# Kernel optimization log

Hardware: AMD Instinct MI355X
Metric: run time of the kernel (lower is better)

The kernel has to match this reference:

```python
import jax, jax.numpy as jnp
import numpy as np

V, E, S, B, T = 100000, 64, 4, 2048, 200
D = 2 * E          # memory_vector_dim
C = E              # controller_units
CIN = 2 * E + D    # controller input: x_t (2E) + prev read (D)
P = 2 * (D + 1) + 2 * D  # (key+beta) for read & write heads + erase + add


def setup_inputs() -> dict:
    key = jax.random.key(0)
    ks = jax.random.split(key, 16)
    g = lambda k, sh, sc=0.05: jax.random.normal(k, sh, dtype=jnp.float32) * sc
    return {
        "item": jax.random.randint(ks[0], (B,), 0, V),
        "cate": jax.random.randint(ks[1], (B,), 0, V),
        "hist_item": jax.random.randint(ks[2], (B, T), 0, V),
        "hist_cate": jax.random.randint(ks[3], (B, T), 0, V),
        "mask": jnp.ones((B, T), jnp.float32),
        "embedding": g(ks[4], (V, E)),
        "gru_Wih": g(ks[5], (3 * C, CIN)),
        "gru_Whh": g(ks[6], (3 * C, C)),
        "gru_bih": jnp.zeros((3 * C,), jnp.float32),
        "gru_bhh": jnp.zeros((3 * C,), jnp.float32),
        "Wp": g(ks[7], (P, C)),
        "bp": jnp.zeros((P,), jnp.float32),
        "Wo": g(ks[8], (E, C + D)),
        "bo": jnp.zeros((E,), jnp.float32),
        "M0": g(ks[9], (S, D), 0.1),
        "fc1_w": g(ks[10], (200, 5 * E)),
        "fc1_b": jnp.zeros((200,), jnp.float32),
        "prelu1_a": jnp.full((1,), 0.25, jnp.float32),
        "fc2_w": g(ks[11], (80, 200)),
        "fc2_b": jnp.zeros((80,), jnp.float32),
        "prelu2_a": jnp.full((1,), 0.25, jnp.float32),
        "fc3_w": g(ks[12], (2, 80)),
        "fc3_b": jnp.zeros((2,), jnp.float32),
    }


def _cos_addr(k, beta, M):
    # content addressing: softmax(beta * cosine_sim(k, M))  k:[B,D] M:[B,S,D]
    kn = k / (jnp.linalg.norm(k, axis=-1, keepdims=True) + 1e-8)
    Mn = M / (jnp.linalg.norm(M, axis=-1, keepdims=True) + 1e-8)
    K = jnp.einsum('bd,bsd->bs', kn, Mn)
    return jax.nn.softmax(beta[:, None] * K, axis=-1)


def _prelu(x, a):
    return jnp.where(x > 0, x, a * x)


def _mimn_rnn(hist_emb, mask, gru_Wih, gru_Whh, gru_bih, gru_bhh, Wp, bp, Wo, bo, M0):
    Bn = hist_emb.shape[0]
    h0 = jnp.zeros((Bn, C), hist_emb.dtype)
    r0 = jnp.zeros((Bn, D), hist_emb.dtype)
    Mi = jnp.broadcast_to(M0[None], (Bn, S, D))

    def step(carry, inp):
        h, M, read = carry
        x_t, m_t = inp                      # x_t [B,2E], m_t [B]
        ctrl_in = jnp.concatenate([x_t, read], axis=-1)
        gi = ctrl_in @ gru_Wih.T + gru_bih
        gh = h @ gru_Whh.T + gru_bhh
        i_r, i_z, i_n = jnp.split(gi, 3, axis=-1)
        h_r, h_z, h_n = jnp.split(gh, 3, axis=-1)
        rg = jax.nn.sigmoid(i_r + h_r)
        zg = jax.nn.sigmoid(i_z + h_z)
        ng = jnp.tanh(i_n + rg * h_n)
        h_new = (1.0 - zg) * ng + zg * h
        # head parameters
        p = h_new @ Wp.T + bp               # [B, P]
        hp_r, hp_w = p[:, :D + 1], p[:, D + 1:2 * (D + 1)]
        erase = jax.nn.sigmoid(p[:, 2 * (D + 1):2 * (D + 1) + D])
        add = jnp.tanh(p[:, -D:])
        k_r, beta_r = jnp.tanh(hp_r[:, :D]), jax.nn.softplus(hp_r[:, D])
        k_w, beta_w = jnp.tanh(hp_w[:, :D]), jax.nn.softplus(hp_w[:, D])
        w_r = _cos_addr(k_r, beta_r, M)
        w_w = _cos_addr(k_w, beta_w, M)
        read_new = jnp.einsum('bs,bsd->bd', w_r, M)
        M_new = M * (1.0 - w_w[..., None] * erase[:, None, :]) + w_w[..., None] * add[:, None, :]
        out = jnp.concatenate([h_new, read_new], axis=-1) @ Wo.T + bo  # [B,E]
        # sequence-length masking (dynamic_rnn semantics)
        v = (m_t > 0)[:, None]
        h = jnp.where(v, h_new, h)
        read = jnp.where(v, read_new, read)
        M = jnp.where(v[..., None], M_new, M)
        out = jnp.where(v, out, jnp.zeros_like(out))
        return (h, M, read), out

    xs = (jnp.swapaxes(hist_emb, 0, 1), jnp.swapaxes(mask, 0, 1))  # [T,B,...]
    _, outs = jax.lax.scan(step, (h0, Mi, r0), xs)
    return jnp.swapaxes(outs, 0, 1)  # [B,T,E]


def reference(item, cate, hist_item, hist_cate, mask, embedding,
              gru_Wih, gru_Whh, gru_bih, gru_bhh, Wp, bp, Wo, bo, M0,
              fc1_w, fc1_b, prelu1_a, fc2_w, fc2_b, prelu2_a, fc3_w, fc3_b):
    item_emb = jnp.concatenate([embedding[item], embedding[cate]], axis=1)      # [B,2E]
    hist_emb = jnp.concatenate([embedding[hist_item], embedding[hist_cate]], axis=2)  # [B,T,2E]
    seq_len = mask.sum(1).astype(jnp.int32)
    outputs = _mimn_rnn(hist_emb, mask, gru_Wih, gru_Whh, gru_bih, gru_bhh, Wp, bp, Wo, bo, M0)
    last_out = jnp.take_along_axis(outputs, (seq_len - 1)[:, None, None], axis=1)[:, 0, :]
    hist_sum = (hist_emb * mask[..., None]).sum(1)                              # [B,2E]
    x = jnp.concatenate([item_emb, hist_sum, last_out], axis=1)                 # [B,5E]
    x = _prelu(x @ fc1_w.T + fc1_b, prelu1_a)
    x = _prelu(x @ fc2_w.T + fc2_b, prelu2_a)
    return x @ fc3_w.T + fc3_b
```

## Files before the change

### kernel.cpp

```cpp
#include <hip/hip_runtime.h>

#define VV 100000
#define BB 2048
#define TT 200
#define GG 192
#define PP 514
#define RPB 8

typedef _Float16 half8 __attribute__((ext_vector_type(8)));
typedef float floatx4 __attribute__((ext_vector_type(4)));
#define MFMA16(a, b, c) __builtin_amdgcn_mfma_f32_16x16x32_f16((a), (b), (c), 0, 0, 0)

#define BARRIER_LDS() do { \
    __asm__ volatile("s_waitcnt lgkmcnt(0)" ::: "memory"); \
    __builtin_amdgcn_s_barrier(); } while (0)

__device__ __forceinline__ float fsigm(float x) { return 1.0f / (1.0f + __expf(-x)); }
__device__ __forceinline__ float ftanh(float x) {
    float e = __expf(2.0f * x);
    return 1.0f - 2.0f / (e + 1.0f);
}
__device__ __forceinline__ float fsoftplus(float x) {
    float e = __expf(-fabsf(x));
    return fmaxf(x, 0.0f) + __logf(1.0f + e);
}

#define DPP_ADD(x, ctrl, rmask) \
    ((x) + __int_as_float(__builtin_amdgcn_update_dpp( \
        0, __float_as_int(x), (ctrl), (rmask), 0xf, true)))
__device__ __forceinline__ float wsum64(float x) {
    x = DPP_ADD(x, 0x111, 0xf);
    x = DPP_ADD(x, 0x112, 0xf);
    x = DPP_ADD(x, 0x114, 0xf);
    x = DPP_ADD(x, 0x118, 0xf);
    x = DPP_ADD(x, 0x142, 0xa);
    x = DPP_ADD(x, 0x143, 0xc);
    return __int_as_float(__builtin_amdgcn_readlane(__float_as_int(x), 63));
}
__device__ __forceinline__ float dot4(float4 w, float4 a) {
    return w.x * a.x + w.y * a.y + w.z * a.z + w.w * a.w;
}

__global__ __launch_bounds__(192) void build_tables(
    const float* __restrict__ emb,
    const float* __restrict__ Wih,
    const float* __restrict__ bih,
    float* __restrict__ GIi, float* __restrict__ GIc)
{
    __shared__ float sE[64 * 64];
    int tid = threadIdx.x;
    int v0 = blockIdx.x * 64;
    for (int i = tid; i < 64 * 64; i += 192) {
        int vv = i >> 6, k = i & 63;
        int gv = v0 + vv;
        sE[i] = (gv < VV) ? emb[(size_t)gv * 64 + k] : 0.0f;
    }
    __syncthreads();
    int n = tid;
    float bi = bih[n];
    {
        float4 w[16];
        const float4* wp = (const float4*)(Wih + n * 256);
#pragma unroll
        for (int q = 0; q < 16; ++q) w[q] = wp[q];
        for (int vv = 0; vv < 64; ++vv) {
            int gv = v0 + vv;
            if (gv >= VV) break;
            const float4* e = (const float4*)&sE[vv * 64];
            float acc = bi;
#pragma unroll
            for (int q = 0; q < 16; ++q) acc += dot4(w[q], e[q]);
            GIi[(size_t)gv * GG + n] = acc;
        }
    }
    {
        float4 w[16];
        const float4* wp = (const float4*)(Wih + n * 256 + 64);
#pragma unroll
        for (int q = 0; q < 16; ++q) w[q] = wp[q];
        for (int vv = 0; vv < 64; ++vv) {
            int gv = v0 + vv;
            if (gv >= VV) break;
            const float4* e = (const float4*)&sE[vv * 64];
            float acc = 0.0f;
#pragma unroll
            for (int q = 0; q < 16; ++q) acc += dot4(w[q], e[q]);
            GIc[(size_t)gv * GG + n] = acc;
        }
    }
}

__global__ __launch_bounds__(128) void hist_stats(
    const int* __restrict__ hist_item, const int* __restrict__ hist_cate,
    const float* __restrict__ mask, const float* __restrict__ emb,
    float* __restrict__ hist_sum, int* __restrict__ seqlen)
{
    int b = blockIdx.x, tid = threadIdx.x;
    const int* hidx = (tid < 64) ? hist_item : hist_cate;
    int j = tid & 63;
    float acc = 0.f;
    for (int t = 0; t < TT; ++t) {
        float m = mask[b * TT + t];
        int idx = hidx[b * TT + t];
        acc += m * emb[(size_t)idx * 64 + j];
    }
    hist_sum[(size_t)b * 128 + tid] = acc;
    if (tid < 64) {
        float s = 0.f;
        for (int t = tid; t < TT; t += 64) s += mask[b * TT + t];
        s = wsum64(s);
        if (tid == 0) seqlen[b] = (int)(s + 0.5f);
    }
}

__global__ __attribute__((amdgpu_flat_work_group_size(512, 512))) void mimn_rnn(
    const int* __restrict__ hist_item, const int* __restrict__ hist_cate,
    const float* __restrict__ mask,
    const float* __restrict__ Wih,
    const float* __restrict__ Whh,
    const float* __restrict__ bhh,
    const float* __restrict__ Wp,
    const float* __restrict__ bp,
    const float* __restrict__ Wo,
    const float* __restrict__ bo,
    const float* __restrict__ M0,
    const float* __restrict__ GIi, const float* __restrict__ GIc,
    const int* __restrict__ seqlen,
    float* __restrict__ last_out)
{
    __shared__ __align__(16) float sU[4160];
    __shared__ __align__(16) _Float16 act16[16 * 200];
    __shared__ __align__(16) _Float16 hn16[16 * 72];
    __shared__ float sHnF[RPB * 64];
    __shared__ float sWpT[2 * 64];
    __shared__ unsigned char sMaskB[RPB * TT];

    const int tid = threadIdx.x;
    const int b0 = blockIdx.x * RPB;
    const int wv = tid >> 6, lane = tid & 63;
    const int nlo = lane & 15, kg = lane >> 4;
    const bool hasN = wv >= 4;

    for (int i = tid; i < 16 * 200; i += 512) act16[i] = (_Float16)0.f;
    for (int i = tid; i < 16 * 72; i += 512) hn16[i] = (_Float16)0.f;
    for (int i = tid; i < RPB * 64; i += 512) sHnF[i] = 0.f;
    if (tid < 128) sWpT[tid] = Wp[512 * 64 + tid];
    for (int i = tid; i < RPB * TT; i += 512) {
        int r = i / TT, tt = i - r * TT;
        sMaskB[i] = (mask[(size_t)(b0 + r) * TT + tt] > 0.f) ? 1 : 0;
    }

    float hreg = 0.f;
    float M1[4], M2[4];
#pragma unroll
    for (int s = 0; s < 4; ++s) {
        M1[s] = M0[s * 128 + lane];
        M2[s] = M0[s * 128 + 64 + lane];
    }
    const float bhhRZ = bhh[16 * wv + nlo];
    const float bhhN  = hasN ? bhh[128 + 16 * (wv - 4) + nlo] : 0.f;
    float bpP[4];
#pragma unroll
    for (int i = 0; i < 4; ++i) bpP[i] = bp[16 * (wv + 8 * i) + nlo];
    const float bpT = (tid < 16) ? bp[512 + (tid >> 3)] : 0.f;

    half8 WG[6];
    {
        int n = 16 * wv + nlo;
#pragma unroll
        for (int kb = 0; kb < 6; ++kb) {
            half8 f;
#pragma unroll
            for (int j = 0; j < 8; ++j) {
                int k = 32 * kb + 8 * kg + j;
                float w = (k < 128) ? Wih[n * 256 + 128 + k] : Whh[n * 64 + (k - 128)];
                f[j] = (_Float16)w;
            }
            WG[kb] = f;
        }
    }
    half8 WN[6];
    if (hasN) {
        int n = 128 + 16 * (wv - 4) + nlo;
#pragma unroll
        for (int kb = 0; kb < 4; ++kb) {
            half8 f;
#pragma unroll
            for (int j = 0; j < 8; ++j) f[j] = (_Float16)Wih[n * 256 + 128 + 32 * kb + 8 * kg + j];
            WN[kb] = f;
        }
#pragma unroll
        for (int kb = 0; kb < 2; ++kb) {
            half8 f;
#pragma unroll
            for (int j = 0; j < 8; ++j) f[j] = (_Float16)Whh[n * 64 + 32 * kb + 8 * kg + j];
            WN[4 + kb] = f;
        }
    } else {
#pragma unroll
        for (int q = 0; q < 6; ++q) WN[q] = half8{};
    }
    half8 WP[8];
#pragma unroll
    for (int i = 0; i < 4; ++i) {
        int n = 16 * (wv + 8 * i) + nlo;
#pragma unroll
        for (int kb = 0; kb < 2; ++kb) {
            half8 f;
#pragma unroll
            for (int j = 0; j < 8; ++j) f[j] = (_Float16)Wp[n * 64 + 32 * kb + 8 * kg + j];
            WP[2 * i + kb] = f;
        }
    }

    int ts = seqlen[b0 + wv] - 1;
    ts = ts < 0 ? 0 : (ts > TT - 1 ? TT - 1 : ts);

    float giA, giB, giC, gcA, gcB, gcC;
    {
        int ri = hist_item[(size_t)(b0 + wv) * TT];
        int rc = hist_cate[(size_t)(b0 + wv) * TT];
        giA = GIi[(size_t)ri * GG + lane];
        giB = GIi[(size_t)ri * GG + 64 + lane];
        giC = GIi[(size_t)ri * GG + 128 + lane];
        gcA = GIc[(size_t)rc * GG + lane];
        gcB = GIc[(size_t)rc * GG + 64 + lane];
        gcC = GIc[(size_t)rc * GG + 128 + lane];
    }
    __syncthreads();

    for (int t = 0; t < TT; ++t) {
        {
            const int abase = nlo * 200 + 8 * kg;
            floatx4 accRZ = {0.f, 0.f, 0.f, 0.f};
            floatx4 accI = {0.f, 0.f, 0.f, 0.f};
            floatx4 accH = {0.f, 0.f, 0.f, 0.f};
            half8 a0 = *(const half8*)&act16[abase];
            half8 a1 = *(const half8*)&act16[abase + 32];
            half8 a2 = *(const half8*)&act16[abase + 64];
            accRZ = MFMA16(a0, WG[0], accRZ);
            accRZ = MFMA16(a1, WG[1], accRZ);
            accRZ = MFMA16(a2, WG[2], accRZ);
            if (hasN) {
                accI = MFMA16(a0, WN[0], accI);
                accI = MFMA16(a1, WN[1], accI);
                accI = MFMA16(a2, WN[2], accI);
            }
            a0 = *(const half8*)&act16[abase + 96];
            a1 = *(const half8*)&act16[abase + 128];
            a2 = *(const half8*)&act16[abase + 160];
            accRZ = MFMA16(a0, WG[3], accRZ);
            accRZ = MFMA16(a1, WG[4], accRZ);
            accRZ = MFMA16(a2, WG[5], accRZ);
            if (hasN) {
                accI = MFMA16(a0, WN[3], accI);
                accH = MFMA16(a1, WN[4], accH);
                accH = MFMA16(a2, WN[5], accH);
            }
            if (kg < 2) {
                int n = 16 * wv + nlo;
#pragma unroll
                for (int q = 0; q < 4; ++q) sU[(4 * kg + q) * 132 + n] = accRZ[q] + bhhRZ;
                if (hasN) {
                    int n64 = 16 * (wv - 4) + nlo;
#pragma unroll
                    for (int q = 0; q < 4; ++q) {
                        sU[1056 + (4 * kg + q) * 68 + n64] = accI[q];
                        sU[1600 + (4 * kg + q) * 68 + n64] = accH[q] + bhhN;
                    }
                }
            }
        }
        BARRIER_LDS();
        bool vld;
        {
            const int r = wv;
            float g_r = sU[r * 132 + lane] + giA + gcA;
            float g_z = sU[r * 132 + 64 + lane] + giB + gcB;
            float i_n = sU[1056 + r * 68 + lane] + giC + gcC;
            float h_n = sU[1600 + r * 68 + lane];
            float rg = fsigm(g_r);
            float zg = fsigm(g_z);
            float ng = ftanh(i_n + rg * h_n);
            float hn = (1.f - zg) * ng + zg * hreg;
            vld = sMaskB[r * TT + t] != 0;
            float hc = vld ? hn : hreg;
            hreg = hc;
            act16[r * 200 + 128 + lane] = (_Float16)hc;
            hn16[r * 72 + lane] = (_Float16)hn;
            sHnF[r * 64 + lane] = hn;
        }
        {
            int tn = (t + 1 < TT) ? t + 1 : TT - 1;
            int ri = hist_item[(size_t)(b0 + wv) * TT + tn];
            int rc = hist_cate[(size_t)(b0 + wv) * TT + tn];
            giA = GIi[(size_t)ri * GG + lane];
            giB = GIi[(size_t)ri * GG + 64 + lane];
            giC = GIi[(size_t)ri * GG + 128 + lane];
            gcA = GIc[(size_t)rc * GG + lane];
            gcB = GIc[(size_t)rc * GG + 64 + lane];
            gcC = GIc[(size_t)rc * GG + 128 + lane];
        }
        BARRIER_LDS();
        {
            const int bbase = nlo * 72 + 8 * kg;
            half8 b0f = *(const half8*)&hn16[bbase];
            half8 b1f = *(const half8*)&hn16[bbase + 32];
#pragma unroll
            for (int i = 0; i < 4; ++i) {
                floatx4 acc = {0.f, 0.f, 0.f, 0.f};
                acc = MFMA16(b0f, WP[2 * i], acc);
                acc = MFMA16(b1f, WP[2 * i + 1], acc);
                if (kg < 2) {
                    int n = 16 * (wv + 8 * i) + nlo;
#pragma unroll
                    for (int q = 0; q < 4; ++q) sU[(4 * kg + q) * 520 + n] = acc[q] + bpP[i];
                }
            }
        }
        if (tid < 16) {
            int r = tid & 7, j = tid >> 3;
            float acc = 0.f;
#pragma unroll
            for (int k = 0; k < 64; ++k) acc += sHnF[r * 64 + k] * sWpT[j * 64 + k];
            sU[r * 520 + 512 + j] = acc + bpT;
        }
        BARRIER_LDS();
        {
            const int row = wv;
            const int pb = row * 520;
#define PV(n) (sU[pb + (n)])
            float kr1 = ftanh(PV(lane)),       kr2 = ftanh(PV(64 + lane));
            float beta_r = fsoftplus(PV(128));
            float kw1 = ftanh(PV(129 + lane)), kw2 = ftanh(PV(193 + lane));
            float beta_w = fsoftplus(PV(257));
            float er1 = fsigm(PV(258 + lane)), er2 = fsigm(PV(322 + lane));
            float ad1 = ftanh(PV(386 + lane)), ad2 = ftanh(PV(450 + lane));
#undef PV
            float nkr = sqrtf(wsum64(kr1 * kr1 + kr2 * kr2)) + 1e-8f;
            float nkw = sqrtf(wsum64(kw1 * kw1 + kw2 * kw2)) + 1e-8f;
            float Kr[4], Kw[4];
#pragma unroll
            for (int s = 0; s < 4; ++s) {
                float nM = sqrtf(wsum64(M1[s] * M1[s] + M2[s] * M2[s])) + 1e-8f;
                float dr = wsum64(kr1 * M1[s] + kr2 * M2[s]);
                float dw = wsum64(kw1 * M1[s] + kw2 * M2[s]);
                Kr[s] = dr / (nkr * nM);
                Kw[s] = dw / (nkw * nM);
            }
            float wr_[4], ww_[4];
            {
                float mx = fmaxf(fmaxf(beta_r * Kr[0], beta_r * Kr[1]),
                                 fmaxf(beta_r * Kr[2], beta_r * Kr[3]));
                float sum = 0.f;
#pragma unroll
                for (int s = 0; s < 4; ++s) { wr_[s] = __expf(beta_r * Kr[s] - mx); sum += wr_[s]; }
                float inv = 1.f / sum;
#pragma unroll
                for (int s = 0; s < 4; ++s) wr_[s] *= inv;
            }
            {
                float mx = fmaxf(fmaxf(beta_w * Kw[0], beta_w * Kw[1]),
                                 fmaxf(beta_w * Kw[2], beta_w * Kw[3]));
                float sum = 0.f;
#pragma unroll
                for (int s = 0; s < 4; ++s) { ww_[s] = __expf(beta_w * Kw[s] - mx); sum += ww_[s]; }
                float inv = 1.f / sum;
#pragma unroll
                for (int s = 0; s < 4; ++s) ww_[s] *= inv;
            }
            float rn1 = 0.f, rn2 = 0.f;
#pragma unroll
            for (int s = 0; s < 4; ++s) { rn1 += wr_[s] * M1[s]; rn2 += wr_[s] * M2[s]; }
            if (vld) {
#pragma unroll
                for (int s = 0; s < 4; ++s) {
                    M1[s] = M1[s] * (1.f - ww_[s] * er1) + ww_[s] * ad1;
                    M2[s] = M2[s] * (1.f - ww_[s] * er2) + ww_[s] * ad2;
                }
                act16[row * 200 + lane]      = (_Float16)rn1;
                act16[row * 200 + 64 + lane] = (_Float16)rn2;
            }
            if (t == ts) {
                float* stash = &sU[pb];
                stash[lane] = rn1; stash[64 + lane] = rn2;
                __asm__ volatile("s_waitcnt lgkmcnt(0)" ::: "memory");
                float acc = bo[lane];
                const float* wo = Wo + lane * GG;
                for (int k = 0; k < 64; ++k)  acc += sHnF[row * 64 + k] * wo[k];
                for (int k = 0; k < 128; ++k) acc += stash[k] * wo[64 + k];
                if (!vld) acc = 0.f;
                last_out[(size_t)(b0 + row) * 64 + lane] = acc;
            }
        }
        BARRIER_LDS();
    }
}

__global__ __launch_bounds__(128) void final_mlp(
    const int* __restrict__ item, const int* __restrict__ cate,
    const float* __restrict__ emb,
    const float* __restrict__ hist_sum, const float* __restrict__ last_out,
    const float* __restrict__ fc1w, const float* __restrict__ fc1b,
    const float* __restrict__ pa1,
    const float* __restrict__ fc2w, const float* __restrict__ fc2b,
    const float* __restrict__ pa2,
    const float* __restrict__ fc3w, const float* __restrict__ fc3b,
    float* __restrict__ out)
{
    __shared__ float sX[320], sH1[200], sH2[80];
    int b = blockIdx.x, tid = threadIdx.x;
    int it = item[b], ct = cate[b];
    for (int i = tid; i < 320; i += 128) {
        float val;
        if (i < 64)       val = emb[(size_t)it * 64 + i];
        else if (i < 128) val = emb[(size_t)ct * 64 + (i - 64)];
        else if (i < 256) val = hist_sum[(size_t)b * 128 + (i - 128)];
        else              val = last_out[(size_t)b * 64 + (i - 256)];
        sX[i] = val;
    }
    __syncthreads();
    float a1 = pa1[0];
    for (int o = tid; o < 200; o += 128) {
        const float4* w = (const float4*)(fc1w + o * 320);
        float acc = fc1b[o];
#pragma unroll
        for (int q = 0; q < 80; ++q) acc += dot4(w[q], *(const float4*)&sX[q * 4]);
        sH1[o] = acc > 0.f ? acc : a1 * acc;
    }
    __syncthreads();
    float a2 = pa2[0];
    for (int o = tid; o < 80; o += 128) {
        const float4* w = (const float4*)(fc2w + o * 200);
        float acc = fc2b[o];
#pragma unroll
        for (int q = 0; q < 50; ++q) acc += dot4(w[q], *(const float4*)&sH1[q * 4]);
        sH2[o] = acc > 0.f ? acc : a2 * acc;
    }
    __syncthreads();
    if (tid < 2) {
        const float4* w = (const float4*)(fc3w + tid * 80);
        float acc = fc3b[tid];
#pragma unroll
        for (int q = 0; q < 20; ++q) acc += dot4(w[q], *(const float4*)&sH2[q * 4]);
        out[b * 2 + tid] = acc;
    }
}

extern "C" void kernel_launch(void* const* d_in, const int* in_sizes, int n_in,
                              void* d_out, int out_size, void* d_ws, size_t ws_size,
                              hipStream_t stream) {
    (void)in_sizes; (void)n_in; (void)out_size; (void)ws_size;
    const int*   item      = (const int*)d_in[0];
    const int*   cate      = (const int*)d_in[1];
    const int*   hist_item = (const int*)d_in[2];
    const int*   hist_cate = (const int*)d_in[3];
    const float* mask = (const float*)d_in[4];
    const float* emb  = (const float*)d_in[5];
    const float* Wih  = (const float*)d_in[6];
    const float* Whh  = (const float*)d_in[7];
    const float* bih  = (const float*)d_in[8];
    const float* bhh  = (const float*)d_in[9];
    const float* Wp   = (const float*)d_in[10];
    const float* bp   = (const float*)d_in[11];
    const float* Wo   = (const float*)d_in[12];
    const float* bo   = (const float*)d_in[13];
    const float* M0   = (const float*)d_in[14];
    const float* fc1w = (const float*)d_in[15];
    const float* fc1b = (const float*)d_in[16];
    const float* pa1  = (const float*)d_in[17];
    const float* fc2w = (const float*)d_in[18];
    const float* fc2b = (const float*)d_in[19];
    const float* pa2  = (const float*)d_in[20];
    const float* fc3w = (const float*)d_in[21];
    const float* fc3b = (const float*)d_in[22];

    float* GIi = (float*)d_ws;
    float* GIc = GIi + (size_t)VV * GG;
    float* hist_sum = GIc + (size_t)VV * GG;
    float* last_out = hist_sum + (size_t)BB * 128;
    int* seqlen = (int*)(last_out + (size_t)BB * 64);

    build_tables<<<(VV + 63) / 64, 192, 0, stream>>>(emb, Wih, bih, GIi, GIc);
    hist_stats<<<BB, 128, 0, stream>>>(hist_item, hist_cate, mask, emb, hist_sum, seqlen);
    mimn_rnn<<<BB / RPB, 512, 0, stream>>>(hist_item, hist_cate, mask, Wih, Whh, bhh,
                                           Wp, bp, Wo, bo, M0, GIi, GIc, seqlen, last_out);
    final_mlp<<<BB, 128, 0, stream>>>(item, cate, emb, hist_sum, last_out,
                                      fc1w, fc1b, pa1, fc2w, fc2b, pa2, fc3w, fc3b,
                                      (float*)d_out);
}
```

Before: 1.270 ms.

## Merge table build and history stats into one MFMA-based prep kernel

Replaces the scalar FP32 dot-product projection table build with fp16 MFMA 16x16x32 tiles, converting embeddings and Wih to half in registers and LDS. The history-sum/seqlen work is folded into the same launch as extra blocks, removing one kernel launch and letting both run concurrently. This lowers the compute cost of the large vocabulary-wide table precompute but adds fp16 rounding to the input-gate table values.

Measured after the change: 1.069 ms. 15.9% less time.

```diff
diff --git a/kernel.cpp b/kernel.cpp
--- a/kernel.cpp
+++ b/kernel.cpp
@@ -6,6 +6,7 @@
 #define GG 192
 #define PP 514
 #define RPB 8
+#define NBT 1563
 
 typedef _Float16 half8 __attribute__((ext_vector_type(8)));
 typedef float floatx4 __attribute__((ext_vector_type(4)));
@@ -41,75 +42,84 @@
     return w.x * a.x + w.y * a.y + w.z * a.z + w.w * a.w;
 }
 
-__global__ __launch_bounds__(192) void build_tables(
+__global__ __launch_bounds__(256) void prep(
     const float* __restrict__ emb,
     const float* __restrict__ Wih,
     const float* __restrict__ bih,
-    float* __restrict__ GIi, float* __restrict__ GIc)
-{
-    __shared__ float sE[64 * 64];
-    int tid = threadIdx.x;
-    int v0 = blockIdx.x * 64;
-    for (int i = tid; i < 64 * 64; i += 192) {
-        int vv = i >> 6, k = i & 63;
-        int gv = v0 + vv;
-        sE[i] = (gv < VV) ? emb[(size_t)gv * 64 + k] : 0.0f;
-    }
-    __syncthreads();
-    int n = tid;
-    float bi = bih[n];
-    {
-        float4 w[16];
-        const float4* wp = (const float4*)(Wih + n * 256);
-#pragma unroll
-        for (int q = 0; q < 16; ++q) w[q] = wp[q];
-        for (int vv = 0; vv < 64; ++vv) {
-            int gv = v0 + vv;
-            if (gv >= VV) break;
-            const float4* e = (const float4*)&sE[vv * 64];
-            float acc = bi;
-#pragma unroll
-            for (int q = 0; q < 16; ++q) acc += dot4(w[q], e[q]);
-            GIi[(size_t)gv * GG + n] = acc;
-        }
-    }
-    {
-        float4 w[16];
-        const float4* wp = (const float4*)(Wih + n * 256 + 64);
-#pragma unroll
-        for (int q = 0; q < 16; ++q) w[q] = wp[q];
-        for (int vv = 0; vv < 64; ++vv) {
-            int gv = v0 + vv;
-            if (gv >= VV) break;
-            const float4* e = (const float4*)&sE[vv * 64];
-            float acc = 0.0f;
-#pragma unroll
-            for (int q = 0; q < 16; ++q) acc += dot4(w[q], e[q]);
-            GIc[(size_t)gv * GG + n] = acc;
-        }
-    }
-}
-
-__global__ __launch_bounds__(128) void hist_stats(
     const int* __restrict__ hist_item, const int* __restrict__ hist_cate,
-    const float* __restrict__ mask, const float* __restrict__ emb,
+    const float* __restrict__ mask,
+    float* __restrict__ GIi, float* __restrict__ GIc,
     float* __restrict__ hist_sum, int* __restrict__ seqlen)
 {
-    int b = blockIdx.x, tid = threadIdx.x;
-    const int* hidx = (tid < 64) ? hist_item : hist_cate;
-    int j = tid & 63;
-    float acc = 0.f;
-    for (int t = 0; t < TT; ++t) {
-        float m = mask[b * TT + t];
-        int idx = hidx[b * TT + t];
-        acc += m * emb[(size_t)idx * 64 + j];
-    }
-    hist_sum[(size_t)b * 128 + tid] = acc;
-    if (tid < 64) {
-        float s = 0.f;
-        for (int t = tid; t < TT; t += 64) s += mask[b * TT + t];
-        s = wsum64(s);
-        if (tid == 0) seqlen[b] = (int)(s + 0.5f);
+    __shared__ __align__(16) _Float16 sE16[64 * 72];
+    const int tid = threadIdx.x;
+    const int wv = tid >> 6, lane = tid & 63;
+    const int nlo = lane & 15, kg = lane >> 4;
+
+    if (blockIdx.x < NBT) {
+        const int v0 = blockIdx.x * 64;
+        for (int i = tid; i < 64 * 64; i += 256) {
+            int vv = i >> 6, k = i & 63;
+            int gv = v0 + vv;
+            sE16[vv * 72 + k] = (gv < VV) ? (_Float16)emb[(size_t)gv * 64 + k]
+                                          : (_Float16)0.f;
+        }
+        half8 WF[6][2];
+        float bias[6];
+#pragma unroll
+        for (int j = 0; j < 6; ++j) {
+            int pid = 6 * wv + j;
+            int tb = pid / 12, nt = pid % 12;
+            int n = nt * 16 + nlo;
+#pragma unroll
+            for (int kb = 0; kb < 2; ++kb) {
+                half8 f;
+#pragma unroll
+                for (int q = 0; q < 8; ++q)
+                    f[q] = (_Float16)Wih[n * 256 + tb * 64 + kb * 32 + kg * 8 + q];
+                WF[j][kb] = f;
+            }
+            bias[j] = tb ? 0.f : bih[n];
+        }
+        __syncthreads();
+#pragma unroll
+        for (int mt = 0; mt < 4; ++mt) {
+            const int ar = (16 * mt + nlo) * 72 + 8 * kg;
+            half8 a0 = *(const half8*)&sE16[ar];
+            half8 a1 = *(const half8*)&sE16[ar + 32];
+#pragma unroll
+            for (int j = 0; j < 6; ++j) {
+                floatx4 acc = {0.f, 0.f, 0.f, 0.f};
+                acc = MFMA16(a0, WF[j][0], acc);
+                acc = MFMA16(a1, WF[j][1], acc);
+                int pid = 6 * wv + j;
+                int tb = pid / 12, nt = pid % 12;
+                float* dst = tb ? GIc : GIi;
+                int n = nt * 16 + nlo;
+#pragma unroll
+                for (int q = 0; q < 4; ++q) {
+                    int gv = v0 + 16 * mt + 4 * kg + q;
+                    if (gv < VV) dst[(size_t)gv * GG + n] = acc[q] + bias[j];
+                }
+            }
+        }
+    } else {
+        const int hb = blockIdx.x - NBT;
+        const int b = hb * 2 + (wv >> 1);
+        const int* hidx = (wv & 1) ? hist_cate : hist_item;
+        float acc = 0.f;
+        for (int t = 0; t < TT; ++t) {
+            float m = mask[(size_t)b * TT + t];
+            int idx = hidx[(size_t)b * TT + t];
+            acc += m * emb[(size_t)idx * 64 + lane];
+        }
+        hist_sum[(size_t)b * 128 + (wv & 1) * 64 + lane] = acc;
+        if ((wv & 1) == 0) {
+            float s = 0.f;
+            for (int t = lane; t < TT; t += 64) s += mask[(size_t)b * TT + t];
+            s = wsum64(s);
+            if (lane == 0) seqlen[b] = (int)(s + 0.5f);
+        }
     }
 }
 
@@ -481,8 +491,8 @@
     float* last_out = hist_sum + (size_t)BB * 128;
     int* seqlen = (int*)(last_out + (size_t)BB * 64);
 
-    build_tables<<<(VV + 63) / 64, 192, 0, stream>>>(emb, Wih, bih, GIi, GIc);
-    hist_stats<<<BB, 128, 0, stream>>>(hist_item, hist_cate, mask, emb, hist_sum, seqlen);
+    prep<<<NBT + BB / 2, 256, 0, stream>>>(emb, Wih, bih, hist_item, hist_cate,
+                                           mask, GIi, GIc, hist_sum, seqlen);
     mimn_rnn<<<BB / RPB, 512, 0, stream>>>(hist_item, hist_cate, mask, Wih, Whh, bhh,
                                            Wp, bp, Wo, bo, M0, GIi, GIc, seqlen, last_out);
     final_mlp<<<BB, 128, 0, stream>>>(item, cate, emb, hist_sum, last_out,
```
